# Optimization experiments

Hardware: AMD Instinct MI355X
Metric: run time of the kernel (lower is better)

The kernel has to match this reference:

```python
import jax, jax.numpy as jnp
import numpy as np
from jax.scipy.special import erf

N_NODES = 128
LAMBDA_MAX = 0.06
EPS = 1e-7


def normal_cdf(x):
    # standard normal CDF, mu=0 sigma2=1
    return 0.5 * (1.0 + erf(x / jnp.sqrt(jnp.asarray(2.0, x.dtype))))


def construct_trajectory(d, c, a, n_nodes):
    """d: [S, N-1], c: [S, N-2], a: [S, N-2, N-1] -> x: [S, N, N-1].

    Sequential recurrence: at each node, QR-orthogonalize the acceleration
    against the previous heading, rotate the heading by angle c, and step by
    distance d. Implemented as lax.scan over nodes (strictly sequential).
    """
    S = d.shape[0]
    D = n_nodes - 1  # effective dim
    e0 = jnp.zeros((S, D), dtype=d.dtype).at[:, 0].set(1.0)  # v_h at node 1
    x1 = d[:, :1] * e0  # x at node 1 (node 0 is origin)

    def step(carry, inp):
        v_prev, x_prev = carry            # [S, D], [S, D]
        a_i, c_i, d_i = inp               # [S, D], [S], [S]
        M = jnp.stack([v_prev, a_i], axis=-1)     # [S, D, 2]
        Q, _ = jnp.linalg.qr(M)                   # batched thin QR
        a_orth = Q[..., 1]                        # orthonormal accel direction
        v = jnp.cos(c_i)[:, None] * v_prev + jnp.sin(c_i)[:, None] * a_orth
        x_new = x_prev + d_i[:, None] * v
        return (v, x_new), x_new

    xs = (jnp.moveaxis(a, 1, 0), c.T, d[:, 1:].T)  # leading axis = N-2 steps
    (_, _), x_rest = jax.lax.scan(step, (e0, x1), xs)  # x_rest: [N-2, S, D]

    x = jnp.concatenate(
        [jnp.zeros((S, 1, D), dtype=d.dtype), x1[:, None, :],
         jnp.moveaxis(x_rest, 0, 1)], axis=1)
    return x  # [S, N, D]


def pairwise_dists(x):
    # x: [S, N, D] -> [S, N, N], via the gram-matrix trick (no [S,N,N,D] blowup)
    sq = jnp.sum(x * x, axis=-1)                         # [S, N]
    gram = jnp.einsum('snd,smd->snm', x, x)              # [S, N, N]
    d2 = sq[:, :, None] + sq[:, None, :] - 2.0 * gram
    return jnp.sqrt(jnp.maximum(d2, 0.0))


def reference(d_raw, c_raw, a_raw, l_raw, all_trials, correct_trials):
    # transforms
    d = jax.nn.softplus(d_raw)                 # rectifier
    c = c_raw                                  # identity
    a = a_raw                                  # identity (orthonormalized later)
    lapse = LAMBDA_MAX * normal_cdf(l_raw)     # [S, 1]

    x = construct_trajectory(d, c, a, N_NODES)         # [S, N, N-1]
    pdists = pairwise_dists(x)                         # [S, N, N]

    sqrt2 = jnp.sqrt(jnp.asarray(2.0, pdists.dtype))
    p_axb = (normal_cdf(pdists / sqrt2) * normal_cdf(pdists / 2.0)
             + normal_cdf(-pdists / sqrt2) * normal_cdf(-pdists / 2.0))
    lam = lapse[:, :, None]                            # [S, 1, 1]
    probs = (1.0 - 2.0 * lam) * p_axb + lam
    probs = jnp.clip(probs, EPS, 1.0 - EPS)

    n_all = all_trials.astype(probs.dtype)[None, :, :]
    n_cor = correct_trials.astype(probs.dtype)[None, :, :]
    ll = n_cor * jnp.log(probs) + (n_all - n_cor) * jnp.log1p(-probs)
    # sum over node pairs, Monte-Carlo mean over samples
    return jnp.mean(jnp.sum(ll, axis=(1, 2)))


def setup_inputs() -> dict:
    key = jax.random.key(0)
    k1, k2, k3, k4, k5, k6 = jax.random.split(key, 6)
    S, N = 2048, N_NODES
    return {
        'd_raw': jax.random.normal(k1, (S, N - 1), dtype=jnp.float32),
        'c_raw': jax.random.normal(k2, (S, N - 2), dtype=jnp.float32),
        'a_raw': jax.random.normal(k3, (S, N - 2, N - 1), dtype=jnp.float32),
        'l_raw': jax.random.normal(k4, (S, 1), dtype=jnp.float32),
        'all_trials': jax.random.randint(k5, (N, N), 0, 80, dtype=jnp.int32),
        'correct_trials': jax.random.randint(k6, (N, N), 0, 40, dtype=jnp.int32),
    }
```

## Files before the change

### kernel.cpp

```cpp
#include <hip/hip_runtime.h>
#include <math.h>

#define S_TOT   2048
#define NNODES  128
#define D_DIM   127
#define N_STEPS 126

typedef unsigned short ushort_t;
typedef unsigned int   uint_t;
typedef __attribute__((ext_vector_type(8))) short bfrag;
typedef __attribute__((ext_vector_type(4))) float f4;

__device__ __forceinline__ float softplus_f(float x) {
    return log1pf(expf(-fabsf(x))) + fmaxf(x, 0.0f);
}
__device__ __forceinline__ float normal_cdf_f(float x) {
    return 0.5f * (1.0f + erff(x * 0.7071067811865475f));
}
__device__ __forceinline__ float frl(float x, int lane) {
    return __int_as_float(__builtin_amdgcn_readlane(__float_as_int(x), lane));
}
__device__ __forceinline__ float wave_sum(float x) {
    float r = x; int v;
    v = __builtin_amdgcn_update_dpp(0, __float_as_int(r), 0x111, 0xf, 0xf, true); r += __int_as_float(v);
    v = __builtin_amdgcn_update_dpp(0, __float_as_int(r), 0x112, 0xf, 0xf, true); r += __int_as_float(v);
    v = __builtin_amdgcn_update_dpp(0, __float_as_int(r), 0x114, 0xf, 0xf, true); r += __int_as_float(v);
    v = __builtin_amdgcn_update_dpp(0, __float_as_int(r), 0x118, 0xf, 0xf, true); r += __int_as_float(v);
    v = __builtin_amdgcn_update_dpp(0, __float_as_int(r), 0x142, 0xa, 0xf, true); r += __int_as_float(v);
    v = __builtin_amdgcn_update_dpp(0, __float_as_int(r), 0x143, 0xc, 0xf, true); r += __int_as_float(v);
    return frl(r, 63);
}
__device__ __forceinline__ ushort_t f2bf(float x) {
    uint_t u = __float_as_uint(x);
    uint_t r = u + 0x7fffu + ((u >> 16) & 1u);
    return (ushort_t)(r >> 16);
}
__device__ __forceinline__ float bf2f(ushort_t h) {
    return __uint_as_float(((uint_t)h) << 16);
}

__global__ __launch_bounds__(256) void prep_counts(
        const int* __restrict__ all_t, const int* __restrict__ cor_t,
        uint_t* __restrict__ pk) {
    int i = blockIdx.x * 256 + threadIdx.x;
    int n = i >> 7, m = i & 127;
    int at = all_t[i], ct = cor_t[i];
    if (n != m) { at += all_t[m * 128 + n]; ct += cor_t[m * 128 + n]; }
    pk[i] = (uint_t)f2bf((float)ct) | ((uint_t)f2bf((float)(at - ct)) << 16);
}

#define LDR1(A, B, row)                                                       \
    { const float* _p = ap + (size_t)(row) * D_DIM + 2 * lane;                \
      A = _p[0];                                                              \
      float _t = _p[d1ok ? 1 : 0];                \
      B = d1ok ? _t : 0.0f; }

#define LOAD_G(BASE, GUARD)                                                   \
    { const int _b = (BASE); const bool _gd = (GUARD);                        \
      if (!_gd || _b + 0  < 126) LDR1(sa0,  sb0,  _b + 0)  else { sa0 = 0; sb0 = 0; }   \
      if (!_gd || _b + 1  < 126) LDR1(sa1,  sb1,  _b + 1)  else { sa1 = 0; sb1 = 0; }   \
      if (!_gd || _b + 2  < 126) LDR1(sa2,  sb2,  _b + 2)  else { sa2 = 0; sb2 = 0; }   \
      if (!_gd || _b + 3  < 126) LDR1(sa3,  sb3,  _b + 3)  else { sa3 = 0; sb3 = 0; }   \
      if (!_gd || _b + 4  < 126) LDR1(sa4,  sb4,  _b + 4)  else { sa4 = 0; sb4 = 0; }   \
      if (!_gd || _b + 5  < 126) LDR1(sa5,  sb5,  _b + 5)  else { sa5 = 0; sb5 = 0; }   \
      if (!_gd || _b + 6  < 126) LDR1(sa6,  sb6,  _b + 6)  else { sa6 = 0; sb6 = 0; }   \
      if (!_gd || _b + 7  < 126) LDR1(sa7,  sb7,  _b + 7)  else { sa7 = 0; sb7 = 0; }   \
      if (!_gd || _b + 8  < 126) LDR1(sa8,  sb8,  _b + 8)  else { sa8 = 0; sb8 = 0; }   \
      if (!_gd || _b + 9  < 126) LDR1(sa9,  sb9,  _b + 9)  else { sa9 = 0; sb9 = 0; }   \
      if (!_gd || _b + 10 < 126) LDR1(sa10, sb10, _b + 10) else { sa10 = 0; sb10 = 0; } \
      if (!_gd || _b + 11 < 126) LDR1(sa11, sb11, _b + 11) else { sa11 = 0; sb11 = 0; } \
      if (!_gd || _b + 12 < 126) LDR1(sa12, sb12, _b + 12) else { sa12 = 0; sb12 = 0; } \
      if (!_gd || _b + 13 < 126) LDR1(sa13, sb13, _b + 13) else { sa13 = 0; sb13 = 0; } \
      if (!_gd || _b + 14 < 126) LDR1(sa14, sb14, _b + 14) else { sa14 = 0; sb14 = 0; } \
      if (!_gd || _b + 15 < 126) LDR1(sa15, sb15, _b + 15) else { sa15 = 0; sb15 = 0; } }

#define WRITE_G(SB)                                                           \
    { const int _s = (SB);                                                    \
      *(float2*)&abuf[_s + 0 ][2 * lane] = make_float2(sa0,  sb0);            \
      *(float2*)&abuf[_s + 1 ][2 * lane] = make_float2(sa1,  sb1);            \
      *(float2*)&abuf[_s + 2 ][2 * lane] = make_float2(sa2,  sb2);            \
      *(float2*)&abuf[_s + 3 ][2 * lane] = make_float2(sa3,  sb3);            \
      *(float2*)&abuf[_s + 4 ][2 * lane] = make_float2(sa4,  sb4);            \
      *(float2*)&abuf[_s + 5 ][2 * lane] = make_float2(sa5,  sb5);            \
      *(float2*)&abuf[_s + 6 ][2 * lane] = make_float2(sa6,  sb6);            \
      *(float2*)&abuf[_s + 7 ][2 * lane] = make_float2(sa7,  sb7);            \
      *(float2*)&abuf[_s + 8 ][2 * lane] = make_float2(sa8,  sb8);            \
      *(float2*)&abuf[_s + 9 ][2 * lane] = make_float2(sa9,  sb9);            \
      *(float2*)&abuf[_s + 10][2 * lane] = make_float2(sa10, sb10);           \
      *(float2*)&abuf[_s + 11][2 * lane] = make_float2(sa11, sb11);           \
      *(float2*)&abuf[_s + 12][2 * lane] = make_float2(sa12, sb12);           \
      *(float2*)&abuf[_s + 13][2 * lane] = make_float2(sa13, sb13);           \
      *(float2*)&abuf[_s + 14][2 * lane] = make_float2(sa14, sb14);           \
      *(float2*)&abuf[_s + 15][2 * lane] = make_float2(sa15, sb15); }

#define STEP_CORE(I, SC, SA, SR, ROWRD, CLSI, DLSI, FLUSH)                    \
    {                                                                         \
        const float ca = ra_r[SC], cb = rb_r[SC];                             \
        float va = wave_sum(fmaf(v0, ca, v1 * cb));                           \
        float ua = fmaf(fmaf(-vp0, aE0U, va), rcp_v, aE0U);                   \
        float w1 = fmaf(-ua, vp1s, aE1U);                                     \
        float inv = __builtin_amdgcn_rsqf(fmaf(-va, va, aaU));                \
        float invs = (w1 >= 0.0f) ? -inv : inv;                               \
        float sf = sU * invs;                                                 \
        float nv0 = fmaf(cU, v0, sf * fmaf(-va, v0, ca));                     \
        float nv1 = fmaf(cU, v1, sf * fmaf(-va, v1, cb));                     \
        float np0 = fmaf(cU, vp0, sf * fmaf(-va, vp0, aE0U));                 \
        float np1 = fmaf(cU, vp1, sf * fmaf(-va, vp1, aE1U));                 \
        v0 = nv0; v1 = nv1; vp0 = np0; vp1 = np1;                             \
        { float ns = copysignf(1.0f, vp0);                                    \
          rcp_v = __builtin_amdgcn_rcpf(vp0 + ns); vp1s = vp1 * ns; }         \
        x0 = fmaf(dU, v0, x0); x1 = fmaf(dU, v1, x1);                         \
        { uint_t pk;                                                          \
          asm("v_cvt_pk_bf16_f32 %0, %1, %2" : "=v"(pk) : "v"(x0), "v"(x1));  \
          xstage[(((I) + 2) & 7) * 64 + lane] = pk; }                         \
        aaU = aa1; aE0U = aE0_1; aE1U = aE1_1; cU = c1; sU = s1; dU = d1;     \
        aa1 = wave_sum(fmaf(ra_r[SA], ra_r[SA], rb_r[SA] * rb_r[SA]));        \
        aE0_1 = frl(ra_r[SA], 0); aE1_1 = frl(rb_r[SA], 0);                   \
        { float2 cs = cls2[CLSI]; c1 = cs.x; s1 = cs.y; }                     \
        d1 = dls[DLSI];                                                       \
        { float2 nx = *(float2*)&abuf[ROWRD][2 * lane];                       \
          ra_r[SR] = nx.x; rb_r[SR] = nx.y; }                                 \
        if (FLUSH) {        \
            uint4 t0 = *(uint4*)&xstage[4 * lane];                            \
            uint4 t1 = *(uint4*)&xstage[256 + 4 * lane];                      \
            uint_t* dst = xg + ((I) - 5) * 64;                                \
            *(uint4*)(dst + 4 * lane) = t0;                                   \
            *(uint4*)(dst + 256 + 4 * lane) = t1;                             \
        }                                                                     \
    }

#define RR(v) ((((v) < 125) ? (v) : 125) & 31)

__global__
__attribute__((amdgpu_flat_work_group_size(64, 64), amdgpu_waves_per_eu(2, 2)))
void traj_kernel(
        const float* __restrict__ d_raw, const float* __restrict__ c_raw,
        const float* __restrict__ a_raw,
        uint_t* __restrict__ xout, int s_base) {
    const int li = blockIdx.x;
    const int s  = s_base + li;
    const int lane = threadIdx.x;
    const bool d1ok = lane < 63;

    __shared__ __align__(16) float abuf[32][128];
    __shared__ __align__(16) uint_t xstage[512];
    __shared__ float  dls[128];
    __shared__ float2 cls2[128];

    float t0 = softplus_f(d_raw[(size_t)s * D_DIM + lane]);
    dls[lane] = t0;
    dls[64 + lane] = d1ok ? softplus_f(d_raw[(size_t)s * D_DIM + 64 + lane]) : 0.0f;
    {
        float cv = c_raw[(size_t)s * N_STEPS + lane];
        cls2[lane] = make_float2(__cosf(cv), __sinf(cv));
        if (lane < 62) {
            float cv2 = c_raw[(size_t)s * N_STEPS + 64 + lane];
            cls2[64 + lane] = make_float2(__cosf(cv2), __sinf(cv2));
        } else {
            cls2[64 + lane] = make_float2(0.0f, 0.0f);
        }
    }

    const float* ap = a_raw + (size_t)s * N_STEPS * D_DIM;
    uint_t* xg = xout + (size_t)li * NNODES * 64;

    float sa0, sa1, sa2, sa3, sa4, sa5, sa6, sa7,
          sa8, sa9, sa10, sa11, sa12, sa13, sa14, sa15;
    float sb0, sb1, sb2, sb3, sb4, sb5, sb6, sb7,
          sb8, sb9, sb10, sb11, sb12, sb13, sb14, sb15;

    LOAD_G(0, false)  WRITE_G(0)
    LOAD_G(16, false) WRITE_G(16)
    LOAD_G(32, false)

    float ra_r[4], rb_r[4];
    { float2 t = *(float2*)&abuf[0][2 * lane]; ra_r[0] = t.x; rb_r[0] = t.y; }
    { float2 t = *(float2*)&abuf[1][2 * lane]; ra_r[1] = t.x; rb_r[1] = t.y; }
    { float2 t = *(float2*)&abuf[2][2 * lane]; ra_r[2] = t.x; rb_r[2] = t.y; }
    ra_r[3] = 0.0f; rb_r[3] = 0.0f;
    float aaU = wave_sum(fmaf(ra_r[0], ra_r[0], rb_r[0] * rb_r[0]));
    float aa1 = wave_sum(fmaf(ra_r[1], ra_r[1], rb_r[1] * rb_r[1]));
    float aE0U = frl(ra_r[0], 0), aE1U = frl(rb_r[0], 0);
    float aE0_1 = frl(ra_r[1], 0), aE1_1 = frl(rb_r[1], 0);
    float cU, sU, c1, s1;
    { float2 cs = cls2[0]; cU = cs.x; sU = cs.y; }
    { float2 cs = cls2[1]; c1 = cs.x; s1 = cs.y; }
    float dU = dls[1], d1 = dls[2];

    float v0 = (lane == 0) ? 1.0f : 0.0f, v1 = 0.0f;
    float vp0 = 1.0f, vp1 = 0.0f, vp1s = 0.0f, rcp_v = 0.5f;
    float x0 = (lane == 0) ? t0 : 0.0f, x1 = 0.0f;

    xstage[lane] = 0u;
    {
        uint_t pk0;
        asm("v_cvt_pk_bf16_f32 %0, %1, %2" : "=v"(pk0) : "v"(x0), "v"(x1));
        xstage[64 + lane] = pk0;
    }

    #pragma unroll 1
    for (int q = 0; q < 31; ++q) {
        const int i0 = q << 2;
        const bool fl = (q & 1) != 0;
        STEP_CORE(i0 + 0, 0, 2, 3, RR(i0 + 3), i0 + 2, i0 + 3, false)
        STEP_CORE(i0 + 1, 1, 3, 0, RR(i0 + 4), i0 + 3, i0 + 4, fl)
        STEP_CORE(i0 + 2, 2, 0, 1, RR(i0 + 5), i0 + 4, i0 + 5, false)
        STEP_CORE(i0 + 3, 3, 1, 2, RR(i0 + 6), i0 + 5, i0 + 6, false)
        if ((q & 3) == 3) {
            const int g = q >> 2;
            if (g <= 5) { WRITE_G((g & 1) << 4) }
            if (g <= 4) LOAD_G((g + 3) << 4, g == 4)
        }
    }
    STEP_CORE(124, 0, 2, 3, 125 & 31, 126, 127, false)
    STEP_CORE(125, 1, 3, 0, 125 & 31, 127, 127, true)
}
#undef RR
#undef STEP_CORE
#undef LOAD_G
#undef WRITE_G
#undef LDR1

__device__ __forceinline__ bfrag ldfrag(const ushort_t* base, int row, int kelem) {
    int byte = ((row << 8) + (kelem << 1)) ^ ((row & 7) << 4);
    return *(const bfrag*)((const char*)base + byte);
}

template<int W>
__device__ __forceinline__ void gram_w(const ushort_t* Xs, f4 (&acc)[9],
                                       int lr, int lg) {
    constexpr int RA = W, RB = 7 - W;
    #pragma unroll
    for (int ks = 0; ks < 4; ++ks) {
        const int kb = ks * 32 + lg * 8;
        const bfrag ha = ldfrag(Xs, RA * 16 + lr, kb);
        const bfrag hb = ldfrag(Xs, RB * 16 + lr, kb);
        #pragma unroll
        for (int TC = W; TC < 8; ++TC) {
            const bfrag bh = ldfrag(Xs, TC * 16 + lr, kb);
            acc[TC - W] = __builtin_amdgcn_mfma_f32_16x16x32_bf16(ha, bh, acc[TC - W], 0, 0, 0);
            if (TC >= RB)
                acc[TC + 1] = __builtin_amdgcn_mfma_f32_16x16x32_bf16(hb, bh, acc[TC + 1], 0, 0, 0);
        }
    }
}

template<int W>
__device__ __forceinline__ void write_sq(const f4 (&acc)[9], float* sq, int lr, int lg) {
    #pragma unroll
    for (int q = 0; q < 4; ++q) {
        if (4 * lg + q == lr) {
            sq[W * 16 + lr]       = acc[0][q];
            sq[(7 - W) * 16 + lr] = acc[8 - W][q];
        }
    }
}

__device__ __forceinline__ float entry_ll(float g, float sqn, float sqm,
        uint_t cw, float lam, float one_m2l) {
    const float d2 = fmaxf(sqn + sqm - 2.0f * g, 0.0f);
    const float pd = __builtin_amdgcn_sqrtf(d2);
    const float A = 0.344f, B = 5.334f, IA = 0.656f, C = 0.3989422804f;
    const float z1 = 0.70710678f * pd, z2 = 0.5f * pd;
    const float e1 = __expf(-0.25f  * d2) * C;
    const float e2 = __expf(-0.125f * d2) * C;
    const float den1 = fmaf(A, __builtin_amdgcn_sqrtf(fmaf(0.5f,  d2, B)), IA * z1);
    const float den2 = fmaf(A, __builtin_amdgcn_sqrtf(fmaf(0.25f, d2, B)), IA * z2);
    const float F1 = e1 * __builtin_amdgcn_rcpf(den1);
    const float F2 = e2 * __builtin_amdgcn_rcpf(den2);
    const float qax = F1 + F2 - 2.0f * F1 * F2;
    float qp = fmaf(one_m2l, qax, lam);
    qp = fminf(fmaxf(qp, 1e-7f), 1.0f - 1e-7f);
    const float pp = 1.0f - qp;
    const float c   = bf2f((ushort_t)(cw & 0xffffu));
    const float amc = bf2f((ushort_t)(cw >> 16));
    return c * __logf(pp) + amc * __logf(qp);
}

__device__ __forceinline__ float tile_ll(f4 a, int TR, int TC, bool diag,
        int lr, int lg, const float* sq, const uint_t* __restrict__ cnt,
        float lam, float one_m2l) {
    float s = 0.0f;
    #pragma unroll
    for (int q = 0; q < 4; ++q) {
        const int n = TR * 16 + 4 * lg + q;
        const int m = TC * 16 + lr;
        if (!diag || (4 * lg + q) <= lr)
            s += entry_ll(a[q], sq[n], sq[m], cnt[n * 128 + m], lam, one_m2l);
    }
    return s;
}

template<int W>
__device__ __forceinline__ float epi(const f4 (&acc)[9], const float* sq,
        const uint_t* __restrict__ cnt, int lr, int lg, float lam, float one_m2l) {
    constexpr int RA = W, RB = 7 - W;
    float s = 0.0f;
    #pragma unroll
    for (int TC = W; TC < 8; ++TC) {
        s += tile_ll(acc[TC - W], RA, TC, (TC == RA), lr, lg, sq, cnt, lam, one_m2l);
        if (TC >= RB)
            s += tile_ll(acc[TC + 1], RB, TC, (TC == RB), lr, lg, sq, cnt, lam, one_m2l);
    }
    return s;
}

__global__ __launch_bounds__(256, 4) void ll_kernel(
        const uint_t* __restrict__ x_g,
        const float* __restrict__ l_raw, const uint_t* __restrict__ cnt,
        float* __restrict__ sums, int s_base) {
    const int li = blockIdx.x;
    const int s  = s_base + li;
    const int t  = threadIdx.x;

    __shared__ __align__(16) ushort_t Xs[NNODES * 128];
    __shared__ float sq[NNODES];
    __shared__ float wsum[4];

    const uint_t* gx = x_g + (size_t)li * NNODES * 64;
    const int l = t & 63, w = t >> 6, lr = l & 15, lg = l >> 4;

    #pragma unroll
    for (int ii = 0; ii < 8; ++ii) {
        const int i = t + ii * 256;
        const int row = i >> 4, j = i & 15;
        const uint4 v = *(const uint4*)(gx + row * 64 + j * 4);
        const int b = ((row << 8) + (j << 4)) ^ ((row & 7) << 4);
        *(uint4*)((char*)Xs + b) = v;
    }
    __syncthreads();

    f4 acc[9];
    #pragma unroll
    for (int i = 0; i < 9; ++i) acc[i] = (f4)(0.0f);

    switch (w) {
        case 0: gram_w<0>(Xs, acc, lr, lg); write_sq<0>(acc, sq, lr, lg); break;
        case 1: gram_w<1>(Xs, acc, lr, lg); write_sq<1>(acc, sq, lr, lg); break;
        case 2: gram_w<2>(Xs, acc, lr, lg); write_sq<2>(acc, sq, lr, lg); break;
        default: gram_w<3>(Xs, acc, lr, lg); write_sq<3>(acc, sq, lr, lg); break;
    }
    __syncthreads();

    const float lam = 0.06f * normal_cdf_f(l_raw[s]);
    const float one_m2l = 1.0f - 2.0f * lam;
    float ll = 0.0f;
    switch (w) {
        case 0: ll = epi<0>(acc, sq, cnt, lr, lg, lam, one_m2l); break;
        case 1: ll = epi<1>(acc, sq, cnt, lr, lg, lam, one_m2l); break;
        case 2: ll = epi<2>(acc, sq, cnt, lr, lg, lam, one_m2l); break;
        default: ll = epi<3>(acc, sq, cnt, lr, lg, lam, one_m2l); break;
    }

    const float wtot = wave_sum(ll);
    if (l == 0) wsum[w] = wtot;
    __syncthreads();
    if (t == 0) sums[s] = wsum[0] + wsum[1] + wsum[2] + wsum[3];
}

__global__ __launch_bounds__(256) void reduce_kernel(
        const float* __restrict__ sums, float* __restrict__ out) {
    __shared__ double sh[256];
    const int t = threadIdx.x;
    double acc = 0.0;
    for (int i = t; i < S_TOT; i += 256) acc += (double)sums[i];
    sh[t] = acc;
    __syncthreads();
    for (int off = 128; off > 0; off >>= 1) {
        if (t < off) sh[t] += sh[t + off];
        __syncthreads();
    }
    if (t == 0) out[0] = (float)(sh[0] / (double)S_TOT);
}

extern "C" void kernel_launch(void* const* d_in, const int* in_sizes, int n_in,
                              void* d_out, int out_size, void* d_ws, size_t ws_size,
                              hipStream_t stream) {
    (void)in_sizes; (void)n_in; (void)out_size;
    const float* d_raw = (const float*)d_in[0];
    const float* c_raw = (const float*)d_in[1];
    const float* a_raw = (const float*)d_in[2];
    const float* l_raw = (const float*)d_in[3];
    const int*   all_t = (const int*)d_in[4];
    const int*   cor_t = (const int*)d_in[5];
    float* out = (float*)d_out;

    char*   ws   = (char*)d_ws;
    float*  sums = (float*)ws;
    uint_t* cnt  = (uint_t*)(ws + 8192);
    char*   xbase = ws + 8192 + 65536;
    const size_t per_sample = (size_t)NNODES * 64 * sizeof(uint_t);

    const size_t head = 8192 + 65536;
    size_t avail = (ws_size > head) ? ws_size - head : 0;
    int chunk = (int)(avail / per_sample);
    if (chunk > S_TOT) chunk = S_TOT;
    if (chunk < 1) chunk = 1;

    prep_counts<<<64, 256, 0, stream>>>(all_t, cor_t, cnt);

    for (int s0 = 0; s0 < S_TOT; s0 += chunk) {
        const int nblk = (S_TOT - s0 < chunk) ? (S_TOT - s0) : chunk;
        uint_t* xbuf = (uint_t*)xbase;
        traj_kernel<<<nblk, 64, 0, stream>>>(d_raw, c_raw, a_raw, xbuf, s0);
        ll_kernel<<<nblk, 256, 0, stream>>>(xbuf, l_raw, cnt, sums, s0);
    }
    reduce_kernel<<<1, 256, 0, stream>>>(sums, out);
}
```

Measured before the change: 100.1 us.

## Precompute acceleration Gram matrix with split-bf16 MFMA to remove per-step wave reductions

Adds a gram_kernel that computes the per-sample Gram matrix of the acceleration rows using hi/lo bf16 splitting on MFMA, stored as fp16. The trajectory kernel becomes a scalar pass that tracks the projections Y = A·v through a linear recurrence on Gram entries, producing per-step (alpha, beta) coefficients, followed by a vector pass that applies them. This removes the serial wave_sum DPP reductions from the sequential critical path. In exchange it adds an extra kernel launch, 32 KB of Gram storage per sample, and fp16 rounding of Gram entries that may cause accuracy drift over 126 steps.

```diff
diff --git a/kernel.cpp b/kernel.cpp
--- a/kernel.cpp
+++ b/kernel.cpp
@@ -38,6 +38,12 @@
 __device__ __forceinline__ float bf2f(ushort_t h) {
     return __uint_as_float(((uint_t)h) << 16);
 }
+__device__ __forceinline__ ushort_t f2h(float x) {
+    return __builtin_bit_cast(ushort_t, (_Float16)x);
+}
+__device__ __forceinline__ float h2f(ushort_t h) {
+    return (float)__builtin_bit_cast(_Float16, h);
+}
 
 __global__ __launch_bounds__(256) void prep_counts(
         const int* __restrict__ all_t, const int* __restrict__ cor_t,
@@ -49,10 +55,115 @@
     pk[i] = (uint_t)f2bf((float)ct) | ((uint_t)f2bf((float)(at - ct)) << 16);
 }
 
+__device__ __forceinline__ bfrag ldfrag(const ushort_t* base, int row, int kelem) {
+    int byte = ((row << 8) + (kelem << 1)) ^ ((row & 7) << 4);
+    return *(const bfrag*)((const char*)base + byte);
+}
+
+template<int W>
+__device__ __forceinline__ void gram3_w(const ushort_t* Hs, const ushort_t* Ls,
+                                        f4 (&acc)[9], int lr, int lg) {
+    constexpr int RA = W, RB = 7 - W;
+    #pragma unroll
+    for (int ks = 0; ks < 4; ++ks) {
+        const int kb = ks * 32 + lg * 8;
+        const bfrag ha = ldfrag(Hs, RA * 16 + lr, kb), la = ldfrag(Ls, RA * 16 + lr, kb);
+        const bfrag hb = ldfrag(Hs, RB * 16 + lr, kb), lb = ldfrag(Ls, RB * 16 + lr, kb);
+        #pragma unroll
+        for (int TC = W; TC < 8; ++TC) {
+            const bfrag ch = ldfrag(Hs, TC * 16 + lr, kb), cl = ldfrag(Ls, TC * 16 + lr, kb);
+            f4& A = acc[TC - W];
+            A = __builtin_amdgcn_mfma_f32_16x16x32_bf16(ha, ch, A, 0, 0, 0);
+            A = __builtin_amdgcn_mfma_f32_16x16x32_bf16(ha, cl, A, 0, 0, 0);
+            A = __builtin_amdgcn_mfma_f32_16x16x32_bf16(la, ch, A, 0, 0, 0);
+            if (TC >= RB) {
+                f4& B = acc[TC + 1];
+                B = __builtin_amdgcn_mfma_f32_16x16x32_bf16(hb, ch, B, 0, 0, 0);
+                B = __builtin_amdgcn_mfma_f32_16x16x32_bf16(hb, cl, B, 0, 0, 0);
+                B = __builtin_amdgcn_mfma_f32_16x16x32_bf16(lb, ch, B, 0, 0, 0);
+            }
+        }
+    }
+}
+
+template<int W>
+__device__ __forceinline__ void store_g(const f4 (&acc)[9], ushort_t* g,
+                                        int lr, int lg) {
+    constexpr int RA = W, RB = 7 - W;
+    #pragma unroll
+    for (int TC = W; TC < 8; ++TC) {
+        #pragma unroll
+        for (int q = 0; q < 4; ++q) {
+            const int m = TC * 16 + lr;
+            const int nA = RA * 16 + 4 * lg + q;
+            g[nA * 128 + m] = f2h(acc[TC - W][q]);
+            if (TC >= RB) {
+                const int nB = RB * 16 + 4 * lg + q;
+                if (nB < 126) g[nB * 128 + m] = f2h(acc[TC + 1][q]);
+            }
+        }
+    }
+}
+
+__global__ __launch_bounds__(256) void gram_kernel(
+        const float* __restrict__ a_raw, ushort_t* __restrict__ G16, int s_base) {
+    const int li = blockIdx.x;
+    const int s  = s_base + li;
+    const int t  = threadIdx.x;
+
+    __shared__ __align__(16) ushort_t Hs[128 * 128];
+    __shared__ __align__(16) ushort_t Ls[128 * 128];
+
+    {
+        uint4* hz = (uint4*)Hs; uint4* lz = (uint4*)Ls;
+        const uint4 z = make_uint4(0u, 0u, 0u, 0u);
+        for (int i = t; i < 2048; i += 256) { hz[i] = z; lz[i] = z; }
+    }
+    __syncthreads();
+
+    const float* ap = a_raw + (size_t)s * 16002;
+    for (int c = t; c < 4001; c += 256) {
+        const int f0 = 4 * c;
+        float2 qa, qb;
+        qa = *(const float2*)(ap + f0);
+        if (c < 4000) qb = *(const float2*)(ap + f0 + 2);
+        else          qb = make_float2(0.0f, 0.0f);
+        #pragma unroll
+        for (int e = 0; e < 4; ++e) {
+            const int f = f0 + e;
+            if (f < 16002) {
+                const int row = (int)(((unsigned)f * 33027u) >> 22);
+                const int col = f - row * 127;
+                const float val = (e == 0) ? qa.x : (e == 1) ? qa.y
+                                : (e == 2) ? qb.x : qb.y;
+                const ushort_t h  = f2bf(val);
+                const ushort_t lo = f2bf(val - bf2f(h));
+                const int off = ((row << 8) + (col << 1)) ^ ((row & 7) << 4);
+                *(ushort_t*)((char*)Hs + off) = h;
+                *(ushort_t*)((char*)Ls + off) = lo;
+            }
+        }
+    }
+    __syncthreads();
+
+    const int l = t & 63, w = t >> 6, lr = l & 15, lg = l >> 4;
+    f4 acc[9];
+    #pragma unroll
+    for (int i = 0; i < 9; ++i) acc[i] = (f4)(0.0f);
+
+    ushort_t* g = G16 + (size_t)li * 16384;
+    switch (w) {
+        case 0: gram3_w<0>(Hs, Ls, acc, lr, lg); store_g<0>(acc, g, lr, lg); break;
+        case 1: gram3_w<1>(Hs, Ls, acc, lr, lg); store_g<1>(acc, g, lr, lg); break;
+        case 2: gram3_w<2>(Hs, Ls, acc, lr, lg); store_g<2>(acc, g, lr, lg); break;
+        default: gram3_w<3>(Hs, Ls, acc, lr, lg); store_g<3>(acc, g, lr, lg); break;
+    }
+}
+
 #define LDR1(A, B, row)                                                       \
     { const float* _p = ap + (size_t)(row) * D_DIM + 2 * lane;                \
       A = _p[0];                                                              \
-      float _t = _p[d1ok ? 1 : 0];                \
+      float _t = _p[d1ok ? 1 : 0];                                            \
       B = d1ok ? _t : 0.0f; }
 
 #define LOAD_G(BASE, GUARD)                                                   \
@@ -93,39 +204,57 @@
       *(float2*)&abuf[_s + 14][2 * lane] = make_float2(sa14, sb14);           \
       *(float2*)&abuf[_s + 15][2 * lane] = make_float2(sa15, sb15); }
 
-#define STEP_CORE(I, SC, SA, SR, ROWRD, CLSI, DLSI, FLUSH)                    \
+#define PSTEP(JV, SC, SR)                                                     \
     {                                                                         \
-        const float ca = ra_r[SC], cb = rb_r[SC];                             \
-        float va = wave_sum(fmaf(v0, ca, v1 * cb));                           \
+        const int j = (JV);                                                   \
+        const float ysel = (j & 1) ? Y1 : Y0;                                 \
+        const float va = __int_as_float(                                      \
+            __builtin_amdgcn_readlane(__float_as_int(ysel), j >> 1));         \
         float ua = fmaf(fmaf(-vp0, aE0U, va), rcp_v, aE0U);                   \
         float w1 = fmaf(-ua, vp1s, aE1U);                                     \
         float inv = __builtin_amdgcn_rsqf(fmaf(-va, va, aaU));                \
         float invs = (w1 >= 0.0f) ? -inv : inv;                               \
         float sf = sU * invs;                                                 \
-        float nv0 = fmaf(cU, v0, sf * fmaf(-va, v0, ca));                     \
-        float nv1 = fmaf(cU, v1, sf * fmaf(-va, v1, cb));                     \
+        float alpha = fmaf(-sf, va, cU);                                      \
+        if (lane == 0) ab_t[j] = make_float2(alpha, sf);                      \
         float np0 = fmaf(cU, vp0, sf * fmaf(-va, vp0, aE0U));                 \
         float np1 = fmaf(cU, vp1, sf * fmaf(-va, vp1, aE1U));                 \
-        v0 = nv0; v1 = nv1; vp0 = np0; vp1 = np1;                             \
+        vp0 = np0; vp1 = np1;                                                 \
         { float ns = copysignf(1.0f, vp0);                                    \
           rcp_v = __builtin_amdgcn_rcpf(vp0 + ns); vp1s = vp1 * ns; }         \
+        { const uint_t gw = gR[SC];                                           \
+          const float g0 = h2f((ushort_t)(gw & 0xffffu));                     \
+          const float g1 = h2f((ushort_t)(gw >> 16));                         \
+          Y0 = fmaf(alpha, Y0, sf * g0);                                      \
+          Y1 = fmaf(alpha, Y1, sf * g1); }                                    \
+        aaU = aa1; aE0U = aE0_1; aE1U = aE1_1; cU = c1; sU = s1;              \
+        aa1 = gdiag[j + 2];                                                   \
+        { float2 e = aEl[j + 2]; aE0_1 = e.x; aE1_1 = e.y; }                  \
+        { float2 cc = cls2[j + 2]; c1 = cc.x; s1 = cc.y; }                    \
+        { const int pr = (j + 3 < 126) ? (j + 3) : 125;                       \
+          gR[SR] = gp[pr * 64 + lane]; }                                      \
+    }
+
+#define ESTEP(I, SC, SR, ROWRD, ABI, DLSI, FLUSH)                             \
+    {                                                                         \
+        const float ca = ra_r[SC], cb = rb_r[SC];                             \
+        v0 = fmaf(aU, v0, bU * ca);                                           \
+        v1 = fmaf(aU, v1, bU * cb);                                           \
         x0 = fmaf(dU, v0, x0); x1 = fmaf(dU, v1, x1);                         \
         { uint_t pk;                                                          \
           asm("v_cvt_pk_bf16_f32 %0, %1, %2" : "=v"(pk) : "v"(x0), "v"(x1));  \
           xstage[(((I) + 2) & 7) * 64 + lane] = pk; }                         \
-        aaU = aa1; aE0U = aE0_1; aE1U = aE1_1; cU = c1; sU = s1; dU = d1;     \
-        aa1 = wave_sum(fmaf(ra_r[SA], ra_r[SA], rb_r[SA] * rb_r[SA]));        \
-        aE0_1 = frl(ra_r[SA], 0); aE1_1 = frl(rb_r[SA], 0);                   \
-        { float2 cs = cls2[CLSI]; c1 = cs.x; s1 = cs.y; }                     \
+        aU = a1n; bU = b1n; dU = d1;                                          \
+        { float2 abv = ab_t[ABI]; a1n = abv.x; b1n = abv.y; }                 \
         d1 = dls[DLSI];                                                       \
         { float2 nx = *(float2*)&abuf[ROWRD][2 * lane];                       \
           ra_r[SR] = nx.x; rb_r[SR] = nx.y; }                                 \
-        if (FLUSH) {        \
-            uint4 t0 = *(uint4*)&xstage[4 * lane];                            \
-            uint4 t1 = *(uint4*)&xstage[256 + 4 * lane];                      \
+        if (FLUSH) {                                                          \
+            uint4 t0v = *(uint4*)&xstage[4 * lane];                           \
+            uint4 t1v = *(uint4*)&xstage[256 + 4 * lane];                     \
             uint_t* dst = xg + ((I) - 5) * 64;                                \
-            *(uint4*)(dst + 4 * lane) = t0;                                   \
-            *(uint4*)(dst + 256 + 4 * lane) = t1;                             \
+            *(uint4*)(dst + 4 * lane) = t0v;                                  \
+            *(uint4*)(dst + 256 + 4 * lane) = t1v;                            \
         }                                                                     \
     }
 
@@ -133,9 +262,9 @@
 
 __global__
 __attribute__((amdgpu_flat_work_group_size(64, 64), amdgpu_waves_per_eu(2, 2)))
-void traj_kernel(
+void scal_kernel(
         const float* __restrict__ d_raw, const float* __restrict__ c_raw,
-        const float* __restrict__ a_raw,
+        const float* __restrict__ a_raw, const ushort_t* __restrict__ G16,
         uint_t* __restrict__ xout, int s_base) {
     const int li = blockIdx.x;
     const int s  = s_base + li;
@@ -146,6 +275,9 @@
     __shared__ __align__(16) uint_t xstage[512];
     __shared__ float  dls[128];
     __shared__ float2 cls2[128];
+    __shared__ float2 ab_t[128];
+    __shared__ float2 aEl[128];
+    __shared__ float  gdiag[128];
 
     float t0 = softplus_f(d_raw[(size_t)s * D_DIM + lane]);
     dls[lane] = t0;
@@ -160,35 +292,73 @@
             cls2[64 + lane] = make_float2(0.0f, 0.0f);
         }
     }
-
     const float* ap = a_raw + (size_t)s * N_STEPS * D_DIM;
-    uint_t* xg = xout + (size_t)li * NNODES * 64;
+    {
+        const float* r0 = ap + (size_t)lane * D_DIM;
+        aEl[lane] = make_float2(r0[0], r0[1]);
+        if (lane < 62) {
+            const float* r1 = ap + (size_t)(64 + lane) * D_DIM;
+            aEl[64 + lane] = make_float2(r1[0], r1[1]);
+        } else {
+            aEl[64 + lane] = make_float2(0.0f, 0.0f);
+        }
+    }
+    const ushort_t* gbase = G16 + (size_t)li * 16384;
+    gdiag[lane] = h2f(gbase[lane * 129]);
+    gdiag[64 + lane] = (lane < 62) ? h2f(gbase[(size_t)(64 + lane) * 129]) : 0.0f;
+    if (lane < 2) ab_t[126 + lane] = make_float2(0.0f, 0.0f);
 
     float sa0, sa1, sa2, sa3, sa4, sa5, sa6, sa7,
           sa8, sa9, sa10, sa11, sa12, sa13, sa14, sa15;
     float sb0, sb1, sb2, sb3, sb4, sb5, sb6, sb7,
           sb8, sb9, sb10, sb11, sb12, sb13, sb14, sb15;
-
     LOAD_G(0, false)  WRITE_G(0)
     LOAD_G(16, false) WRITE_G(16)
     LOAD_G(32, false)
 
+    const uint_t* gp = (const uint_t*)gbase;
+    uint_t gR[4];
+    gR[0] = gp[0 * 64 + lane];
+    gR[1] = gp[1 * 64 + lane];
+    gR[2] = gp[2 * 64 + lane];
+    gR[3] = 0u;
+
+    float Y0 = aEl[2 * lane].x;
+    float Y1 = aEl[2 * lane + 1].x;
+    float vp0 = 1.0f, vp1 = 0.0f, vp1s = 0.0f, rcp_v = 0.5f;
+    float cU, sU, c1, s1;
+    { float2 cc = cls2[0]; cU = cc.x; sU = cc.y; }
+    { float2 cc = cls2[1]; c1 = cc.x; s1 = cc.y; }
+    float aaU = gdiag[0], aa1 = gdiag[1];
+    float aE0U, aE1U, aE0_1, aE1_1;
+    { float2 e = aEl[0]; aE0U = e.x; aE1U = e.y; }
+    { float2 e = aEl[1]; aE0_1 = e.x; aE1_1 = e.y; }
+
+    #pragma unroll 1
+    for (int q2 = 0; q2 < 31; ++q2) {
+        const int jb = q2 << 2;
+        PSTEP(jb + 0, 0, 3)
+        PSTEP(jb + 1, 1, 0)
+        PSTEP(jb + 2, 2, 1)
+        PSTEP(jb + 3, 3, 2)
+    }
+    PSTEP(124, 0, 3)
+    PSTEP(125, 1, 0)
+
+    uint_t* xg = xout + (size_t)li * NNODES * 64;
+
     float ra_r[4], rb_r[4];
-    { float2 t = *(float2*)&abuf[0][2 * lane]; ra_r[0] = t.x; rb_r[0] = t.y; }
-    { float2 t = *(float2*)&abuf[1][2 * lane]; ra_r[1] = t.x; rb_r[1] = t.y; }
-    { float2 t = *(float2*)&abuf[2][2 * lane]; ra_r[2] = t.x; rb_r[2] = t.y; }
+    { float2 tv = *(float2*)&abuf[0][2 * lane]; ra_r[0] = tv.x; rb_r[0] = tv.y; }
+    { float2 tv = *(float2*)&abuf[1][2 * lane]; ra_r[1] = tv.x; rb_r[1] = tv.y; }
+    { float2 tv = *(float2*)&abuf[2][2 * lane]; ra_r[2] = tv.x; rb_r[2] = tv.y; }
     ra_r[3] = 0.0f; rb_r[3] = 0.0f;
-    float aaU = wave_sum(fmaf(ra_r[0], ra_r[0], rb_r[0] * rb_r[0]));
-    float aa1 = wave_sum(fmaf(ra_r[1], ra_r[1], rb_r[1] * rb_r[1]));
-    float aE0U = frl(ra_r[0], 0), aE1U = frl(rb_r[0], 0);
-    float aE0_1 = frl(ra_r[1], 0), aE1_1 = frl(rb_r[1], 0);
-    float cU, sU, c1, s1;
-    { float2 cs = cls2[0]; cU = cs.x; sU = cs.y; }
-    { float2 cs = cls2[1]; c1 = cs.x; s1 = cs.y; }
+
+    float aU, bU, a1n, b1n;
+    { float2 abv = ab_t[0]; aU = abv.x; bU = abv.y; }
+    { float2 abv = ab_t[1]; a1n = abv.x; b1n = abv.y; }
     float dU = dls[1], d1 = dls[2];
 
     float v0 = (lane == 0) ? 1.0f : 0.0f, v1 = 0.0f;
-    float vp0 = 1.0f, vp1 = 0.0f, vp1s = 0.0f, rcp_v = 0.5f;
     float x0 = (lane == 0) ? t0 : 0.0f, x1 = 0.0f;
 
     xstage[lane] = 0u;
@@ -202,29 +372,25 @@
     for (int q = 0; q < 31; ++q) {
         const int i0 = q << 2;
         const bool fl = (q & 1) != 0;
-        STEP_CORE(i0 + 0, 0, 2, 3, RR(i0 + 3), i0 + 2, i0 + 3, false)
-        STEP_CORE(i0 + 1, 1, 3, 0, RR(i0 + 4), i0 + 3, i0 + 4, fl)
-        STEP_CORE(i0 + 2, 2, 0, 1, RR(i0 + 5), i0 + 4, i0 + 5, false)
-        STEP_CORE(i0 + 3, 3, 1, 2, RR(i0 + 6), i0 + 5, i0 + 6, false)
+        ESTEP(i0 + 0, 0, 3, RR(i0 + 3), i0 + 2, i0 + 3, false)
+        ESTEP(i0 + 1, 1, 0, RR(i0 + 4), i0 + 3, i0 + 4, fl)
+        ESTEP(i0 + 2, 2, 1, RR(i0 + 5), i0 + 4, i0 + 5, false)
+        ESTEP(i0 + 3, 3, 2, RR(i0 + 6), i0 + 5, i0 + 6, false)
         if ((q & 3) == 3) {
             const int g = q >> 2;
             if (g <= 5) { WRITE_G((g & 1) << 4) }
             if (g <= 4) LOAD_G((g + 3) << 4, g == 4)
         }
     }
-    STEP_CORE(124, 0, 2, 3, 125 & 31, 126, 127, false)
-    STEP_CORE(125, 1, 3, 0, 125 & 31, 127, 127, true)
-}
+    ESTEP(124, 0, 3, 125 & 31, 126, 127, false)
+    ESTEP(125, 1, 0, 125 & 31, 127, 127, true)
+}
+#undef PSTEP
+#undef ESTEP
 #undef RR
-#undef STEP_CORE
 #undef LOAD_G
 #undef WRITE_G
 #undef LDR1
-
-__device__ __forceinline__ bfrag ldfrag(const ushort_t* base, int row, int kelem) {
-    int byte = ((row << 8) + (kelem << 1)) ^ ((row & 7) << 4);
-    return *(const bfrag*)((const char*)base + byte);
-}
 
 template<int W>
 __device__ __forceinline__ void gram_w(const ushort_t* Xs, f4 (&acc)[9],
@@ -389,7 +555,7 @@
     float*  sums = (float*)ws;
     uint_t* cnt  = (uint_t*)(ws + 8192);
     char*   xbase = ws + 8192 + 65536;
-    const size_t per_sample = (size_t)NNODES * 64 * sizeof(uint_t);
+    const size_t per_sample = 65536;
 
     const size_t head = 8192 + 65536;
     size_t avail = (ws_size > head) ? ws_size - head : 0;
@@ -401,8 +567,10 @@
 
     for (int s0 = 0; s0 < S_TOT; s0 += chunk) {
         const int nblk = (S_TOT - s0 < chunk) ? (S_TOT - s0) : chunk;
-        uint_t* xbuf = (uint_t*)xbase;
-        traj_kernel<<<nblk, 64, 0, stream>>>(d_raw, c_raw, a_raw, xbuf, s0);
+        uint_t*   xbuf = (uint_t*)xbase;
+        ushort_t* G16  = (ushort_t*)(xbase + (size_t)chunk * 32768);
+        gram_kernel<<<nblk, 256, 0, stream>>>(a_raw, G16, s0);
+        scal_kernel<<<nblk, 64, 0, stream>>>(d_raw, c_raw, a_raw, G16, xbuf, s0);
         ll_kernel<<<nblk, 256, 0, stream>>>(xbuf, l_raw, cnt, sums, s0);
     }
     reduce_kernel<<<1, 256, 0, stream>>>(sums, out);
```

Measured after the change: 193.1 us. 1.93x slower.
